# Kernel optimization log

Measured on AMD Instinct MI355X. Metric: run time of the kernel, lower is better.

## Reference

```python
import jax, jax.numpy as jnp
import numpy as np

N_NODES = 50000
N_EDGES = 800000
ATOM_DIM = 128
BOND_DIM = 16
HID = 128
STEPS = 4


def setup_inputs() -> dict:
    key = jax.random.key(0)
    k1, k2, k3, k4, k5, k6 = jax.random.split(key, 6)
    atoms = jax.random.normal(k1, (N_NODES, ATOM_DIM), dtype=jnp.float32)
    bonds = jax.random.normal(k2, (N_NODES, BOND_DIM), dtype=jnp.float32)
    pairs = jax.random.randint(k3, (N_EDGES, 2), 0, N_NODES)
    # sort rows by target id (tf.math.segment_sum expects sorted segment ids)
    order = jnp.argsort(pairs[:, 0])
    pairs = pairs[order].astype(jnp.int64)
    # learned parameters (glorot-ish scaling)
    kernel = jax.random.normal(k4, (ATOM_DIM, BOND_DIM * BOND_DIM), dtype=jnp.float32) * (2.0 / (ATOM_DIM + BOND_DIM * BOND_DIM)) ** 0.5
    bias = jnp.zeros((BOND_DIM * BOND_DIM,), dtype=jnp.float32)
    weight_node = jax.random.normal(k5, (BOND_DIM, HID), dtype=jnp.float32) * (2.0 / (BOND_DIM + HID)) ** 0.5
    weight_node_inp = jax.random.normal(k6, (BOND_DIM, HID), dtype=jnp.float32) * (2.0 / (BOND_DIM + HID)) ** 0.5
    return {"atoms": atoms, "bonds": bonds, "pairs": pairs,
            "kernel": kernel, "bias": bias,
            "weight_node": weight_node, "weight_node_inp": weight_node_inp}


def reference(atoms, bonds, pairs, kernel, bias, weight_node, weight_node_inp):
    n, bd = bonds.shape
    # per-node transform -> [N, bd, bd] message matrices
    A = (atoms @ kernel + bias).reshape(n, bd, bd)
    src = pairs[:, 0]
    nbr = pairs[:, 1]
    # gather bonds of neighbors, apply source-node matrix per edge: [E, bd]
    trans = jnp.einsum('eij,ej->ei', A[src], bonds[nbr])
    # scatter-add back to nodes keyed on pairs[:,0]
    aggregate = jax.ops.segment_sum(trans, src, num_segments=n)  # [N, bd]
    # step loop: aggregate is never updated in the original, so each step
    # computes the identical result; compute once and replicate.
    nodes = aggregate @ weight_node            # [N, hid]
    edges = jax.nn.relu(bonds @ weight_node_inp)  # [N, hid]
    result = jax.nn.relu(nodes + edges)
    return jnp.stack([result] * STEPS)  # [steps, N, hid]
```

## Files before the change

kernel.cpp:

```cpp
#include <hip/hip_runtime.h>

typedef __attribute__((ext_vector_type(8))) short bf16x8;
typedef __attribute__((ext_vector_type(4))) float f32x4;

constexpr int N       = 50000;
constexpr int NE      = 800000;
constexpr int AD      = 128;
constexpr int BD      = 16;
constexpr int BD2     = 256;
constexpr int HIDDEN  = 128;
constexpr int EPG     = 32;
constexpr int NB      = 64;

__device__ inline short f2bf(float f) {
    union U { float f; unsigned u; } v; v.f = f;
    unsigned r = v.u + 0x7fffu + ((v.u >> 16) & 1u);
    return (short)(r >> 16);
}

__global__ __launch_bounds__(256) void prep_kbf(
    const float* __restrict__ kmat, short* __restrict__ kbf)
{
    int t = blockIdx.x * 256 + threadIdx.x;
    int u = t >> 6, l = t & 63;
    int nf = u >> 2, kk = u & 3;
    int col = nf * 16 + (l & 15);
    int k0  = kk * 32 + (l >> 4) * 8;
    bf16x8 o;
#pragma unroll
    for (int j = 0; j < 8; ++j) o[j] = f2bf(kmat[(size_t)(k0 + j) * BD2 + col]);
    *(bf16x8*)(kbf + (size_t)t * 8) = o;
}

__global__ __launch_bounds__(256) void edge_scatter_sorted(
    const int2* __restrict__ pairs,
    const float* __restrict__ bonds,
    float* __restrict__ S)
{
    const int gid = (int)((blockIdx.x * (unsigned)blockDim.x + threadIdx.x) >> 4);
    const int c   = threadIdx.x & 15;
    long e0 = (long)gid * EPG;
    if (e0 >= NE) return;

    int   cur = -1;
    float acc = 0.f;
    for (long e = e0; e < e0 + EPG; e += 4) {
        int2 pb[4]; float vb[4];
#pragma unroll
        for (int i = 0; i < 4; ++i) pb[i] = pairs[e + i];
#pragma unroll
        for (int i = 0; i < 4; ++i) vb[i] = bonds[(size_t)pb[i].y * BD + c];
#pragma unroll
        for (int i = 0; i < 4; ++i) {
            if (pb[i].x != cur) {
                if (cur >= 0) atomicAdd(&S[(size_t)cur * BD + c], acc);
                acc = 0.f;
                cur = pb[i].x;
            }
            acc += vb[i];
        }
    }
    atomicAdd(&S[(size_t)cur * BD + c], acc);
}

__global__ __launch_bounds__(256, 3) void fused_node_mfma(
    const float* __restrict__ atoms,
    const float* __restrict__ bonds,
    const short* __restrict__ kbf,
    const float* __restrict__ bias,
    const float* __restrict__ Wn,
    const float* __restrict__ Wi,
    const float* __restrict__ S,
    float* __restrict__ out)
{
    __shared__ float wn_lds[16 * 128];
    __shared__ float wi_lds[16 * 128];
    __shared__ float bonds_lds[NB * 20];
    __shared__ float agg_lds[NB * 17];

    const int tid = threadIdx.x;
    const int nb  = blockIdx.x * NB;

    {
#pragma unroll
        for (int p = 0; p < 2; ++p) {
            int i4 = (tid + 256 * p) * 4;
            *(float4*)(wn_lds + i4) = *(const float4*)(Wn + i4);
            *(float4*)(wi_lds + i4) = *(const float4*)(Wi + i4);
        }
        int row = tid >> 2, j4 = (tid & 3) * 4;
        int n = nb + row; if (n >= N) n = N - 1;
        *(float4*)(bonds_lds + row * 20 + j4) = *(const float4*)(bonds + (size_t)n * BD + j4);
    }

    const int w  = tid >> 6;
    const int l  = tid & 63;
    const int lq = l >> 4;
    const int lj = l & 15;
    const int wrow = nb + w * 16;

    int arow = wrow + lj; if (arow >= N) arow = N - 1;
    const float* ap = atoms + (size_t)arow * AD + lq * 8;
    bf16x8 afrag[4];
#pragma unroll
    for (int kk = 0; kk < 4; ++kk) {
        float4 a0 = *(const float4*)(ap + kk * 32);
        float4 a1 = *(const float4*)(ap + kk * 32 + 4);
        bf16x8 af;
        af[0] = f2bf(a0.x); af[1] = f2bf(a0.y); af[2] = f2bf(a0.z); af[3] = f2bf(a0.w);
        af[4] = f2bf(a1.x); af[5] = f2bf(a1.y); af[6] = f2bf(a1.z); af[7] = f2bf(a1.w);
        afrag[kk] = af;
    }

    f32x4 acc[16];
#pragma unroll
    for (int nf = 0; nf < 16; ++nf) acc[nf] = (f32x4){0.f, 0.f, 0.f, 0.f};

    const bf16x8* kb = (const bf16x8*)kbf;
#pragma unroll 1
    for (int kk = 0; kk < 4; ++kk) {
#pragma unroll
        for (int nf = 0; nf < 16; ++nf) {
            bf16x8 b = kb[(size_t)(nf * 4 + kk) * 64 + l];
            acc[nf] = __builtin_amdgcn_mfma_f32_16x16x32_bf16(afrag[kk], b, acc[nf], 0, 0, 0);
        }
    }

    float sval[4];
#pragma unroll
    for (int r = 0; r < 4; ++r) {
        int n = wrow + 4 * lq + r; if (n >= N) n = N - 1;
        sval[r] = S[(size_t)n * BD + lj];
    }
    float aggv[4];
#pragma unroll
    for (int nf = 0; nf < 16; ++nf) {
        float bv = bias[nf * 16 + lj];
#pragma unroll
        for (int r = 0; r < 4; ++r) {
            float p = (acc[nf][r] + bv) * sval[r];
            p += __shfl_xor(p, 1);
            p += __shfl_xor(p, 2);
            p += __shfl_xor(p, 4);
            p += __shfl_xor(p, 8);
            if (lj == nf) aggv[r] = p;
        }
    }
#pragma unroll
    for (int r = 0; r < 4; ++r)
        agg_lds[(w * 16 + 4 * lq + r) * 17 + lj] = aggv[r];

    __syncthreads();

    {
        const int r2 = tid >> 2;
        const int hg = tid & 3;
        const int n2 = nb + r2;
        float aggr[16], bvr[16];
#pragma unroll
        for (int i = 0; i < 16; ++i) {
            aggr[i] = agg_lds[r2 * 17 + i];
            bvr[i]  = bonds_lds[r2 * 20 + i];
        }
        if (n2 < N) {
#pragma unroll
            for (int hv = 0; hv < 8; ++hv) {
                int h = (hv * 4 + hg) * 4;
                float4 nv = make_float4(0.f, 0.f, 0.f, 0.f);
                float4 ev = make_float4(0.f, 0.f, 0.f, 0.f);
#pragma unroll
                for (int i = 0; i < 16; ++i) {
                    float4 wv  = *(const float4*)(wn_lds + i * 128 + h);
                    float4 wv2 = *(const float4*)(wi_lds + i * 128 + h);
                    nv.x = fmaf(aggr[i], wv.x, nv.x);
                    nv.y = fmaf(aggr[i], wv.y, nv.y);
                    nv.z = fmaf(aggr[i], wv.z, nv.z);
                    nv.w = fmaf(aggr[i], wv.w, nv.w);
                    ev.x = fmaf(bvr[i], wv2.x, ev.x);
                    ev.y = fmaf(bvr[i], wv2.y, ev.y);
                    ev.z = fmaf(bvr[i], wv2.z, ev.z);
                    ev.w = fmaf(bvr[i], wv2.w, ev.w);
                }
                ev.x = fmaxf(ev.x, 0.f); ev.y = fmaxf(ev.y, 0.f);
                ev.z = fmaxf(ev.z, 0.f); ev.w = fmaxf(ev.w, 0.f);
                float4 rv;
                rv.x = fmaxf(nv.x + ev.x, 0.f);
                rv.y = fmaxf(nv.y + ev.y, 0.f);
                rv.z = fmaxf(nv.z + ev.z, 0.f);
                rv.w = fmaxf(nv.w + ev.w, 0.f);
#pragma unroll
                for (int s = 0; s < 4; ++s) {
                    *(float4*)(out + ((size_t)s * N + n2) * HIDDEN + h) = rv;
                }
            }
        }
    }
}

extern "C" void kernel_launch(void* const* d_in, const int* in_sizes, int n_in,
                              void* d_out, int out_size, void* d_ws, size_t ws_size,
                              hipStream_t stream)
{
    const float* atoms = (const float*)d_in[0];
    const float* bonds = (const float*)d_in[1];
    const int2*  pairs = (const int2*)d_in[2];
    const float* kmat  = (const float*)d_in[3];
    const float* bias  = (const float*)d_in[4];
    const float* Wn    = (const float*)d_in[5];
    const float* Wi    = (const float*)d_in[6];
    float* out = (float*)d_out;

    float* S   = (float*)d_ws;
    short* kbf = (short*)((char*)d_ws + (size_t)N * BD * 4);

    hipMemsetAsync(S, 0, (size_t)N * BD * sizeof(float), stream);
    prep_kbf<<<16, 256, 0, stream>>>(kmat, kbf);

    const int groups  = NE / EPG;
    const int threads = groups * 16;
    edge_scatter_sorted<<<(threads + 255) / 256, 256, 0, stream>>>(pairs, bonds, S);

    fused_node_mfma<<<(N + NB - 1) / NB, 256, 0, stream>>>(
        atoms, bonds, kbf, bias, Wn, Wi, S, out);
}
```

Measured before the change: 78.53 us.

## Move node/edge output projections onto MFMA and drop LDS staging

```diff
diff --git a/kernel.cpp b/kernel.cpp
--- a/kernel.cpp
+++ b/kernel.cpp
@@ -18,18 +18,38 @@
     return (short)(r >> 16);
 }
 
-__global__ __launch_bounds__(256) void prep_kbf(
-    const float* __restrict__ kmat, short* __restrict__ kbf)
+__global__ __launch_bounds__(256) void prep_frags(
+    const float* __restrict__ kmat,
+    const float* __restrict__ Wn,
+    const float* __restrict__ Wi,
+    short* __restrict__ kbf,
+    short* __restrict__ wbf)
 {
     int t = blockIdx.x * 256 + threadIdx.x;
-    int u = t >> 6, l = t & 63;
-    int nf = u >> 2, kk = u & 3;
-    int col = nf * 16 + (l & 15);
-    int k0  = kk * 32 + (l >> 4) * 8;
-    bf16x8 o;
-#pragma unroll
-    for (int j = 0; j < 8; ++j) o[j] = f2bf(kmat[(size_t)(k0 + j) * BD2 + col]);
-    *(bf16x8*)(kbf + (size_t)t * 8) = o;
+    if (t < 4096) {
+        int u = t >> 6, l = t & 63;
+        int nf = u >> 2, kk = u & 3;
+        int col = nf * 16 + (l & 15);
+        int k0  = kk * 32 + (l >> 4) * 8;
+        bf16x8 o;
+#pragma unroll
+        for (int j = 0; j < 8; ++j) o[j] = f2bf(kmat[(size_t)(k0 + j) * BD2 + col]);
+        *(bf16x8*)(kbf + (size_t)t * 8) = o;
+    } else if (t < 4096 + 1024) {
+        int t2 = t - 4096;
+        int u = t2 >> 6, l = t2 & 63;
+        int m = u >> 3, nf2 = u & 7;
+        const float* W = m ? Wi : Wn;
+        int col = nf2 * 16 + (l & 15);
+        int k0  = (l >> 4) * 8;
+        bf16x8 o;
+#pragma unroll
+        for (int j = 0; j < 8; ++j) {
+            int k = k0 + j;
+            o[j] = (k < 16) ? f2bf(W[(size_t)k * HIDDEN + col]) : (short)0;
+        }
+        *(bf16x8*)(wbf + (size_t)t2 * 8) = o;
+    }
 }
 
 __global__ __launch_bounds__(256) void edge_scatter_sorted(
@@ -67,37 +87,17 @@
     const float* __restrict__ atoms,
     const float* __restrict__ bonds,
     const short* __restrict__ kbf,
+    const short* __restrict__ wbf,
     const float* __restrict__ bias,
-    const float* __restrict__ Wn,
-    const float* __restrict__ Wi,
     const float* __restrict__ S,
     float* __restrict__ out)
 {
-    __shared__ float wn_lds[16 * 128];
-    __shared__ float wi_lds[16 * 128];
-    __shared__ float bonds_lds[NB * 20];
-    __shared__ float agg_lds[NB * 17];
-
     const int tid = threadIdx.x;
-    const int nb  = blockIdx.x * NB;
-
-    {
-#pragma unroll
-        for (int p = 0; p < 2; ++p) {
-            int i4 = (tid + 256 * p) * 4;
-            *(float4*)(wn_lds + i4) = *(const float4*)(Wn + i4);
-            *(float4*)(wi_lds + i4) = *(const float4*)(Wi + i4);
-        }
-        int row = tid >> 2, j4 = (tid & 3) * 4;
-        int n = nb + row; if (n >= N) n = N - 1;
-        *(float4*)(bonds_lds + row * 20 + j4) = *(const float4*)(bonds + (size_t)n * BD + j4);
-    }
-
-    const int w  = tid >> 6;
-    const int l  = tid & 63;
-    const int lq = l >> 4;
-    const int lj = l & 15;
-    const int wrow = nb + w * 16;
+    const int w   = tid >> 6;
+    const int l   = tid & 63;
+    const int lq  = l >> 4;
+    const int lj  = l & 15;
+    const int wrow = blockIdx.x * NB + w * 16;
 
     int arow = wrow + lj; if (arow >= N) arow = N - 1;
     const float* ap = atoms + (size_t)arow * AD + lq * 8;
@@ -122,76 +122,57 @@
 #pragma unroll
         for (int nf = 0; nf < 16; ++nf) {
             bf16x8 b = kb[(size_t)(nf * 4 + kk) * 64 + l];
-            acc[nf] = __builtin_amdgcn_mfma_f32_16x16x32_bf16(afrag[kk], b, acc[nf], 0, 0, 0);
-        }
-    }
-
-    float sval[4];
-#pragma unroll
-    for (int r = 0; r < 4; ++r) {
-        int n = wrow + 4 * lq + r; if (n >= N) n = N - 1;
-        sval[r] = S[(size_t)n * BD + lj];
-    }
-    float aggv[4];
+            acc[nf] = __builtin_amdgcn_mfma_f32_16x16x32_bf16(b, afrag[kk], acc[nf], 0, 0, 0);
+        }
+    }
+
+    int srow = wrow + lj; if (srow >= N) srow = N - 1;
+    float4 sv = *(const float4*)(S + (size_t)srow * BD + lq * 4);
+
+    float aggf[16];
 #pragma unroll
     for (int nf = 0; nf < 16; ++nf) {
-        float bv = bias[nf * 16 + lj];
+        float4 bv = *(const float4*)(bias + nf * 16 + lq * 4);
+        float q = (acc[nf][0] + bv.x) * sv.x
+                + (acc[nf][1] + bv.y) * sv.y
+                + (acc[nf][2] + bv.z) * sv.z
+                + (acc[nf][3] + bv.w) * sv.w;
+        q += __shfl_xor(q, 16);
+        q += __shfl_xor(q, 32);
+        aggf[nf] = q;
+    }
+
+    bf16x8 agg_a = (bf16x8){0,0,0,0,0,0,0,0};
+    bf16x8 bond_a = (bf16x8){0,0,0,0,0,0,0,0};
+    if (lq < 2) {
+#pragma unroll
+        for (int j = 0; j < 8; ++j) agg_a[j] = f2bf(aggf[lq * 8 + j]);
+        int brow = wrow + lj; if (brow >= N) brow = N - 1;
+        float4 b0 = *(const float4*)(bonds + (size_t)brow * BD + lq * 8);
+        float4 b1 = *(const float4*)(bonds + (size_t)brow * BD + lq * 8 + 4);
+        bond_a[0] = f2bf(b0.x); bond_a[1] = f2bf(b0.y); bond_a[2] = f2bf(b0.z); bond_a[3] = f2bf(b0.w);
+        bond_a[4] = f2bf(b1.x); bond_a[5] = f2bf(b1.y); bond_a[6] = f2bf(b1.z); bond_a[7] = f2bf(b1.w);
+    }
+
+    const bf16x8* wb = (const bf16x8*)wbf;
+#pragma unroll
+    for (int nf2 = 0; nf2 < 8; ++nf2) {
+        bf16x8 wn_f = wb[(size_t)nf2 * 64 + l];
+        bf16x8 wi_f = wb[(size_t)(8 + nf2) * 64 + l];
+        f32x4 e = __builtin_amdgcn_mfma_f32_16x16x32_bf16(
+            bond_a, wi_f, (f32x4){0.f, 0.f, 0.f, 0.f}, 0, 0, 0);
+        e[0] = fmaxf(e[0], 0.f); e[1] = fmaxf(e[1], 0.f);
+        e[2] = fmaxf(e[2], 0.f); e[3] = fmaxf(e[3], 0.f);
+        f32x4 o = __builtin_amdgcn_mfma_f32_16x16x32_bf16(agg_a, wn_f, e, 0, 0, 0);
 #pragma unroll
         for (int r = 0; r < 4; ++r) {
-            float p = (acc[nf][r] + bv) * sval[r];
-            p += __shfl_xor(p, 1);
-            p += __shfl_xor(p, 2);
-            p += __shfl_xor(p, 4);
-            p += __shfl_xor(p, 8);
-            if (lj == nf) aggv[r] = p;
-        }
-    }
-#pragma unroll
-    for (int r = 0; r < 4; ++r)
-        agg_lds[(w * 16 + 4 * lq + r) * 17 + lj] = aggv[r];
-
-    __syncthreads();
-
-    {
-        const int r2 = tid >> 2;
-        const int hg = tid & 3;
-        const int n2 = nb + r2;
-        float aggr[16], bvr[16];
-#pragma unroll
-        for (int i = 0; i < 16; ++i) {
-            aggr[i] = agg_lds[r2 * 17 + i];
-            bvr[i]  = bonds_lds[r2 * 20 + i];
-        }
-        if (n2 < N) {
-#pragma unroll
-            for (int hv = 0; hv < 8; ++hv) {
-                int h = (hv * 4 + hg) * 4;
-                float4 nv = make_float4(0.f, 0.f, 0.f, 0.f);
-                float4 ev = make_float4(0.f, 0.f, 0.f, 0.f);
-#pragma unroll
-                for (int i = 0; i < 16; ++i) {
-                    float4 wv  = *(const float4*)(wn_lds + i * 128 + h);
-                    float4 wv2 = *(const float4*)(wi_lds + i * 128 + h);
-                    nv.x = fmaf(aggr[i], wv.x, nv.x);
-                    nv.y = fmaf(aggr[i], wv.y, nv.y);
-                    nv.z = fmaf(aggr[i], wv.z, nv.z);
-                    nv.w = fmaf(aggr[i], wv.w, nv.w);
-                    ev.x = fmaf(bvr[i], wv2.x, ev.x);
-                    ev.y = fmaf(bvr[i], wv2.y, ev.y);
-                    ev.z = fmaf(bvr[i], wv2.z, ev.z);
-                    ev.w = fmaf(bvr[i], wv2.w, ev.w);
-                }
-                ev.x = fmaxf(ev.x, 0.f); ev.y = fmaxf(ev.y, 0.f);
-                ev.z = fmaxf(ev.z, 0.f); ev.w = fmaxf(ev.w, 0.f);
-                float4 rv;
-                rv.x = fmaxf(nv.x + ev.x, 0.f);
-                rv.y = fmaxf(nv.y + ev.y, 0.f);
-                rv.z = fmaxf(nv.z + ev.z, 0.f);
-                rv.w = fmaxf(nv.w + ev.w, 0.f);
-#pragma unroll
-                for (int s = 0; s < 4; ++s) {
-                    *(float4*)(out + ((size_t)s * N + n2) * HIDDEN + h) = rv;
-                }
+            int node = wrow + 4 * lq + r;
+            if (node < N) {
+                float v = fmaxf(o[r], 0.f);
+                size_t base = (size_t)node * HIDDEN + nf2 * 16 + lj;
+#pragma unroll
+                for (int s = 0; s < 4; ++s)
+                    out[base + (size_t)s * N * HIDDEN] = v;
             }
         }
     }
@@ -212,14 +193,15 @@
 
     float* S   = (float*)d_ws;
     short* kbf = (short*)((char*)d_ws + (size_t)N * BD * 4);
+    short* wbf = kbf + 4096 * 8;
 
     hipMemsetAsync(S, 0, (size_t)N * BD * sizeof(float), stream);
-    prep_kbf<<<16, 256, 0, stream>>>(kmat, kbf);
+    prep_frags<<<20, 256, 0, stream>>>(kmat, Wn, Wi, kbf, wbf);
 
     const int groups  = NE / EPG;
     const int threads = groups * 16;
     edge_scatter_sorted<<<(threads + 255) / 256, 256, 0, stream>>>(pairs, bonds, S);
 
     fused_node_mfma<<<(N + NB - 1) / NB, 256, 0, stream>>>(
-        atoms, bonds, kbf, bias, Wn, Wi, S, out);
-}
+        atoms, bonds, kbf, wbf, bias, S, out);
+}
```

Result: faster. 71.91 us (-8.4%).
